# Kernel tuning notes

Measured on AMD Instinct MI355X. Metric: run time of the kernel, lower is better.

The kernel has to match this reference:

```python
import jax, jax.numpy as jnp
import numpy as np

# SofthebbArgs constants (rate, adaptive=True, p, dot_uw=False, temp)
RATE = 1e-3
TEMP = 1.0
P = 0.5


def negate_non_maximal(t):
    # keep the per-row max entry, negate all others
    idx = jnp.argmax(t, axis=-1)                      # [B]
    mask = idx[:, None] == jnp.arange(t.shape[-1])    # [B, OUT]
    return jnp.where(mask, t, -t)


def setup_inputs() -> dict:
    key = jax.random.key(0)
    k1, k2 = jax.random.split(key, 2)
    B, IN, OUT = 8192, 1024, 1024
    x = jax.random.normal(k1, (B, IN), dtype=jnp.float32)
    # xavier_normal_ with gain=1: std = sqrt(2/(fan_in+fan_out))
    W = jax.random.normal(k2, (OUT, IN), dtype=jnp.float32) * (2.0 / (IN + OUT)) ** 0.5
    b = jnp.zeros((OUT,), dtype=jnp.float32)
    return {"x": x, "W": W, "b": b}


def reference(x, W, b):
    # --- HebbianLinear.forward (act = Identity) ---
    u = x @ W.T + b                                   # [B, OUT]
    y = u
    # --- softhebb: y = softmax(y / temp), then _hebb with dot_uw=False ---
    ysm = jax.nn.softmax(y / TEMP, axis=1)
    yn = negate_non_maximal(ysm)                      # [B, OUT]
    Bn = x.shape[0]
    # _hebb materializes dw[b,o,i] = yn[b,o]*(x[b,i] - u[b,o]*W[o,i]) then means over b.
    # Algebraically fused (no [B,OUT,IN] intermediate):
    #   step[o,i] = (yn^T x)[o,i]/B - mean_b(yn[b,o]*u[b,o]) * W[o,i]
    step = (yn.T @ x) / Bn - jnp.mean(yn * u, axis=0)[:, None] * W  # [OUT, IN]
    # adaptive per-row rate: rate * |1 - ||W_row||_2|^p
    diff = jnp.abs(1.0 - jnp.linalg.norm(W, axis=1))  # [OUT]
    rate = RATE * diff ** P
    return rate[:, None] * step                       # [OUT, IN]
```

## Files before the change

kernel.cpp:

```cpp
#include <hip/hip_runtime.h>

#define BATCH 8192
#define INF_  1024
#define OUTF  1024
#define INV_B (1.0f/8192.0f)
#define RATE_C 1e-3f
#define SPLITZ 8

typedef __bf16 bf16x8 __attribute__((ext_vector_type(8)));
typedef float  f32x4  __attribute__((ext_vector_type(4)));
typedef float  f32x16 __attribute__((ext_vector_type(16)));
typedef const __attribute__((address_space(1))) unsigned int* gas_t;
typedef __attribute__((address_space(3))) unsigned int* las_t;

static __device__ __forceinline__ unsigned short f2bf(float f) {
  unsigned int u = __float_as_uint(f);
  u += 0x7fffu + ((u >> 16) & 1u);
  return (unsigned short)(u >> 16);
}
static __device__ __forceinline__ float bf2f(unsigned short h) {
  return __uint_as_float(((unsigned int)h) << 16);
}

__global__ __launch_bounds__(256) void k_convert(
    const float* __restrict__ x, unsigned short* __restrict__ xb,
    unsigned short* __restrict__ xT, const float* __restrict__ W,
    unsigned short* __restrict__ Wb, float* __restrict__ rate) {
  const int t = threadIdx.x;
  if (blockIdx.x >= 2048) {
    __shared__ float red[256];
    const int o = blockIdx.x - 2048;
    float4 v = *(const float4*)&W[(size_t)o * INF_ + t * 4];
    ushort4 h;
    h.x = f2bf(v.x); h.y = f2bf(v.y); h.z = f2bf(v.z); h.w = f2bf(v.w);
    *(ushort4*)&Wb[(size_t)o * INF_ + t * 4] = h;
    red[t] = v.x * v.x + v.y * v.y + v.z * v.z + v.w * v.w;
    __syncthreads();
    for (int s = 128; s > 0; s >>= 1) {
      if (t < s) red[t] += red[t + s];
      __syncthreads();
    }
    if (t == 0) {
      float nrm = sqrtf(red[0]);
      rate[o] = RATE_C * sqrtf(fabsf(1.0f - nrm));
    }
    return;
  }
  __shared__ unsigned int t32[64][33];
  const int bx = blockIdx.x & 15;
  const int by = blockIdx.x >> 4;
  const int r0 = by * 64;
  const int c0 = bx * 64;
  const int m = t & 15;
  const int q = t >> 4;
#pragma unroll
  for (int p = 0; p < 2; ++p) {
    const int r2 = p * 16 + q;
    const int b  = r0 + 2 * r2;
    float4 v0 = *(const float4*)&x[(size_t)b * INF_ + c0 + 4 * m];
    float4 v1 = *(const float4*)&x[(size_t)(b + 1) * INF_ + c0 + 4 * m];
    ushort4 h0, h1;
    h0.x = f2bf(v0.x); h0.y = f2bf(v0.y); h0.z = f2bf(v0.z); h0.w = f2bf(v0.w);
    h1.x = f2bf(v1.x); h1.y = f2bf(v1.y); h1.z = f2bf(v1.z); h1.w = f2bf(v1.w);
    *(ushort4*)&xb[(size_t)b * INF_ + c0 + 4 * m] = h0;
    *(ushort4*)&xb[(size_t)(b + 1) * INF_ + c0 + 4 * m] = h1;
    t32[4 * m + 0][r2] = (unsigned int)h0.x | ((unsigned int)h1.x << 16);
    t32[4 * m + 1][r2] = (unsigned int)h0.y | ((unsigned int)h1.y << 16);
    t32[4 * m + 2][r2] = (unsigned int)h0.z | ((unsigned int)h1.z << 16);
    t32[4 * m + 3][r2] = (unsigned int)h0.w | ((unsigned int)h1.w << 16);
  }
  __syncthreads();
  const int c  = t >> 2;
  const int sg = t & 3;
  unsigned int vb[8];
#pragma unroll
  for (int k = 0; k < 8; ++k) vb[k] = t32[c][sg * 8 + k];
  unsigned short* dst = &xT[(size_t)(c0 + c) * BATCH + r0 + sg * 16];
  *(uint4*)&dst[0] = make_uint4(vb[0], vb[1], vb[2], vb[3]);
  *(uint4*)&dst[8] = make_uint4(vb[4], vb[5], vb[6], vb[7]);
}

__global__ __launch_bounds__(256, 3) void k_gemm(
    const unsigned short* __restrict__ A, const unsigned short* __restrict__ B,
    int lda, int ldb, int kChunk, void* __restrict__ C, int ldc,
    const float* __restrict__ bias, int mode) {
  __shared__ unsigned short smem[128 * 132];
  unsigned short* As = smem;
  unsigned short* Bs = smem + 128 * 64;
  const int t  = threadIdx.x;
  const int id = blockIdx.x;
  int bx, by, bz;
  if (mode == 0) {
    by = (id & 7) | ((id >> 6) << 3);
    bx = (id >> 3) & 7;
    bz = 0;
  } else {
    bz = id & 7;
    by = (id >> 3) & 7;
    bx = (id >> 6) & 7;
  }
  const int m0   = by * 128;
  const int n0   = bx * 128;
  const int k0   = bz * kChunk;
  const int lane = t & 63;
  const int wave = t >> 6;
  const int sr   = lane >> 3;
  const int scx  = ((lane & 7) ^ sr) * 8;
  const int wm   = (wave >> 1) * 64;
  const int wn   = (wave & 1) * 64;
  const int fm   = lane & 31;
  const int fh   = lane >> 5;

  f32x16 acc[2][2] = {};

  const int ldsRow0 = wave * 8;
  const size_t gArow = (size_t)(m0 + ldsRow0 + sr) * lda + scx;
  const size_t gBrow = (size_t)(n0 + ldsRow0 + sr) * ldb + scx;

  for (int ks = 0; ks < kChunk; ks += 64) {
    const int k = k0 + ks;
#pragma unroll
    for (int j = 0; j < 4; ++j) {
      __builtin_amdgcn_global_load_lds(
          (gas_t)&A[gArow + (size_t)j * 32 * lda + k],
          (las_t)&As[(ldsRow0 + j * 32) * 64], 16, 0, 0);
      __builtin_amdgcn_global_load_lds(
          (gas_t)&B[gBrow + (size_t)j * 32 * ldb + k],
          (las_t)&Bs[(ldsRow0 + j * 32) * 64], 16, 0, 0);
    }
    __syncthreads();
#pragma unroll
    for (int kk = 0; kk < 64; kk += 16) {
      const int ckk = (kk >> 3) + fh;
      const int swz = (ckk ^ (lane & 7)) << 3;
      bf16x8 af[2], bf[2];
#pragma unroll
      for (int i = 0; i < 2; ++i)
        af[i] = *(const bf16x8*)&As[(wm + i * 32 + fm) * 64 + swz];
#pragma unroll
      for (int i = 0; i < 2; ++i)
        bf[i] = *(const bf16x8*)&Bs[(wn + i * 32 + fm) * 64 + swz];
#pragma unroll
      for (int mt = 0; mt < 2; ++mt)
#pragma unroll
        for (int nt = 0; nt < 2; ++nt)
          acc[mt][nt] = __builtin_amdgcn_mfma_f32_32x32x16_bf16(
              af[mt], bf[nt], acc[mt][nt], 0, 0, 0);
    }
    __syncthreads();
  }

#pragma unroll
  for (int nt = 0; nt < 2; ++nt) {
    const int cc = wn + nt * 32 + fm;
    const float bv = (mode == 0) ? bias[n0 + cc] : 0.0f;
#pragma unroll
    for (int mt = 0; mt < 2; ++mt) {
#pragma unroll
      for (int r = 0; r < 16; ++r) {
        const int rr = wm + mt * 32 + (r & 3) + 8 * (r >> 2) + 4 * fh;
        smem[rr * 132 + cc] = f2bf(acc[mt][nt][r] + bv);
      }
    }
  }
  __syncthreads();
  unsigned short* Cb = (mode == 0)
      ? (unsigned short*)C
      : (unsigned short*)C + (size_t)bz * (1024u * 1024u);
#pragma unroll
  for (int i = 0; i < 8; ++i) {
    const int row = i * 16 + (t >> 4);
    const int ch  = (t & 15) * 8;
    const unsigned short* src = &smem[row * 132 + ch];
    unsigned short* dst = &Cb[(size_t)(m0 + row) * ldc + n0 + ch];
    *(uint2*)&dst[0] = *(const uint2*)&src[0];
    *(uint2*)&dst[4] = *(const uint2*)&src[4];
  }
}

__global__ __launch_bounds__(256) void k_row_stats(
    const unsigned short* __restrict__ ub, const float* __restrict__ x,
    const float* __restrict__ W, float* __restrict__ rowmax,
    float* __restrict__ rowinv, int* __restrict__ rowarg) {
  __shared__ int cands[4][32];
  __shared__ int cnt[4];
  const int lane = threadIdx.x & 63;
  const int wave = threadIdx.x >> 6;
  const int b    = blockIdx.x * 4 + wave;
  const int oBase = lane * 16;

  float a[16];
  {
    uint4 q0 = *(const uint4*)&ub[(size_t)b * OUTF + oBase];
    uint4 q1 = *(const uint4*)&ub[(size_t)b * OUTF + oBase + 8];
    const unsigned int* qa = (const unsigned int*)&q0;
    const unsigned int* qb = (const unsigned int*)&q1;
#pragma unroll
    for (int c = 0; c < 4; ++c) {
      a[2 * c]         = __uint_as_float(qa[c] << 16);
      a[2 * c + 1]     = __uint_as_float(qa[c] & 0xffff0000u);
      a[8 + 2 * c]     = __uint_as_float(qb[c] << 16);
      a[8 + 2 * c + 1] = __uint_as_float(qb[c] & 0xffff0000u);
    }
  }
  float mv = a[0]; int mi = oBase;
#pragma unroll
  for (int j = 1; j < 16; ++j)
    if (a[j] > mv) { mv = a[j]; mi = oBase + j; }
#pragma unroll
  for (int off = 1; off < 64; off <<= 1) {
    float ov = __shfl_xor(mv, off);
    int   oi = __shfl_xor(mi, off);
    if (ov > mv || (ov == mv && oi < mi)) { mv = ov; mi = oi; }
  }
  const float M = mv;
  float se = 0.0f;
#pragma unroll
  for (int j = 0; j < 16; ++j) se += __expf(a[j] - M);
#pragma unroll
  for (int off = 1; off < 64; off <<= 1) se += __shfl_xor(se, off);

  const float thr = M - 0.10f;
  unsigned int cflags = 0;
  int ccount = 0;
#pragma unroll
  for (int j = 0; j < 16; ++j)
    if (a[j] >= thr) { cflags |= (1u << j); ++ccount; }
  int tot = ccount;
#pragma unroll
  for (int off = 1; off < 64; off <<= 1) tot += __shfl_xor(tot, off);

  int best = mi;
  if (tot > 1) {
    if (lane == 0) cnt[wave] = 0;
    for (int j = 0; j < 16; ++j)
      if (cflags & (1u << j)) {
        int p = atomicAdd(&cnt[wave], 1);
        if (p < 32) cands[wave][p] = oBase + j;
      }
    int nc = cnt[wave]; if (nc > 32) nc = 32;
    float xr[16];
    const float* xp = &x[(size_t)b * INF_ + oBase];
#pragma unroll
    for (int j = 0; j < 16; j += 4) {
      float4 v = *(const float4*)&xp[j];
      xr[j] = v.x; xr[j + 1] = v.y; xr[j + 2] = v.z; xr[j + 3] = v.w;
    }
    float bv = -3.4e38f; int bi = 0x7fffffff;
    for (int c = 0; c < nc; ++c) {
      const int o = cands[wave][c];
      const float* wp = &W[(size_t)o * INF_ + oBase];
      float d = 0.0f;
#pragma unroll
      for (int j = 0; j < 16; j += 4) {
        float4 v = *(const float4*)&wp[j];
        d += xr[j] * v.x + xr[j + 1] * v.y + xr[j + 2] * v.z +
             xr[j + 3] * v.w;
      }
#pragma unroll
      for (int off = 1; off < 64; off <<= 1) d += __shfl_xor(d, off);
      if (d > bv || (d == bv && o < bi)) { bv = d; bi = o; }
    }
    best = bi;
  }
  if (lane == 0) {
    rowmax[b] = M;
    rowinv[b] = 1.0f / se;
    rowarg[b] = best;
  }
}

__global__ __launch_bounds__(256) void k_yn(
    const unsigned short* __restrict__ ub, const float* __restrict__ rowmax,
    const float* __restrict__ rowinv, const int* __restrict__ rowarg,
    unsigned short* __restrict__ ynT, float* __restrict__ s_part) {
  __shared__ unsigned short tile[256][72];
  __shared__ float smax[64], sinv[64];
  __shared__ int   sarg[64];
  const int t  = threadIdx.x;
  const int o0 = blockIdx.x * 256;
  const int b0 = blockIdx.y * 64;
  if (t < 64) {
    smax[t] = rowmax[b0 + t];
    sinv[t] = rowinv[b0 + t];
    sarg[t] = rowarg[b0 + t];
  }
  __syncthreads();
  const int o = o0 + t;
  float sacc = 0.0f;
#pragma unroll
  for (int g = 0; g < 8; ++g) {
    uint4 pkv;
    unsigned short* pk = (unsigned short*)&pkv;
#pragma unroll
    for (int j = 0; j < 8; ++j) {
      const int r = g * 8 + j;
      float uu  = bf2f(ub[(size_t)(b0 + r) * OUTF + o]);
      float ysm = __expf(uu - smax[r]) * sinv[r];
      float yn  = (o == sarg[r]) ? ysm : -ysm;
      sacc += yn * uu;
      pk[j] = f2bf(yn);
    }
    *(uint4*)&tile[t][g * 8] = pkv;
  }
  s_part[(size_t)blockIdx.y * OUTF + o] = sacc;
  __syncthreads();
#pragma unroll
  for (int it = 0; it < 8; ++it) {
    const int row = it * 32 + (t >> 3);
    const int seg = (t & 7) * 8;
    uint4 vv = *(const uint4*)&tile[row][seg];
    *(uint4*)&ynT[(size_t)(o0 + row) * BATCH + b0 + seg] = vv;
  }
}

__global__ __launch_bounds__(256) void k_final(
    const unsigned short* __restrict__ Cp, const float* __restrict__ W,
    const float* __restrict__ s_part, const float* __restrict__ rate,
    float* __restrict__ out) {
  __shared__ float sred[128];
  const int t  = threadIdx.x;
  const int id = blockIdx.x;
  const int o  = ((id & 7) << 7) | (id >> 3);
  if (t < 128) sred[t] = s_part[(size_t)t * OUTF + o];
  __syncthreads();
  for (int s2 = 64; s2 > 0; s2 >>= 1) {
    if (t < s2) sred[t] += sred[t + s2];
    __syncthreads();
  }
  const float sb = sred[0] * INV_B;
  const float rt = rate[o];
  const int i0 = t * 4;
  float cx = 0, cy = 0, cz = 0, cw = 0;
#pragma unroll
  for (int z = 0; z < SPLITZ; ++z) {
    ushort4 h = *(const ushort4*)&Cp[(size_t)z * (1024u * 1024u) +
                                     (size_t)o * INF_ + i0];
    cx += bf2f(h.x); cy += bf2f(h.y); cz += bf2f(h.z); cw += bf2f(h.w);
  }
  float4 w = *(const float4*)&W[(size_t)o * INF_ + i0];
  float4 r;
  r.x = rt * (cx * INV_B - sb * w.x);
  r.y = rt * (cy * INV_B - sb * w.y);
  r.z = rt * (cz * INV_B - sb * w.z);
  r.w = rt * (cw * INV_B - sb * w.w);
  *(float4*)&out[(size_t)o * INF_ + i0] = r;
}

extern "C" void kernel_launch(void* const* d_in, const int* in_sizes, int n_in,
                              void* d_out, int out_size, void* d_ws, size_t ws_size,
                              hipStream_t stream) {
  const float* x    = (const float*)d_in[0];
  const float* W    = (const float*)d_in[1];
  const float* bias = (const float*)d_in[2];
  float* out = (float*)d_out;
  char* ws = (char*)d_ws;

  unsigned short* ub    = (unsigned short*)(ws + 0);
  unsigned short* xb    = (unsigned short*)(ws + 16777216);
  unsigned short* xT    = (unsigned short*)(ws + 33554432);
  unsigned short* ynT   = (unsigned short*)(ws + 50331648);
  unsigned short* Wb    = (unsigned short*)(ws + 67108864);
  float*          rate  = (float*)(ws + 69206016);
  float*          spart = (float*)(ws + 69210112);
  float*          rmax  = (float*)(ws + 69734400);
  float*          rinv  = (float*)(ws + 69767168);
  int*            rarg  = (int*)  (ws + 69799936);

  k_convert<<<dim3(3072), 256, 0, stream>>>(x, xb, xT, W, Wb, rate);
  k_gemm<<<dim3(512), 256, 0, stream>>>(xb, Wb, 1024, 1024, 1024,
                                        ub, 1024, bias, 0);
  k_row_stats<<<dim3(2048), 256, 0, stream>>>(ub, x, W, rmax, rinv, rarg);
  k_yn<<<dim3(4, 128), 256, 0, stream>>>(ub, rmax, rinv, rarg, ynT, spart);
  k_gemm<<<dim3(512), 256, 0, stream>>>(ynT, xT, 8192, 8192, 1024,
                                        ws, 1024, nullptr, 1);
  k_final<<<dim3(1024), 256, 0, stream>>>((const unsigned short*)ws, W, spart,
                                          rate, out);
}
```

Measured before the change: 153.6 us.

## Double-buffer LDS tiles in bf16 GEMM to overlap global loads with MFMA

The GEMM kernel now keeps two LDS buffers for the A/B tiles. It issues the global-to-LDS loads for the next K step right after the barrier, while MFMAs run on the current buffer. This removes one barrier per iteration and hides load latency behind compute. In exchange, LDS use per block doubles and the launch bound drops from 3 to 2 blocks per CU, which may lower occupancy. The epilogue staging area now spans both buffers.

Result: no change. 151.9 us, median of 2 (-1.1%).

```diff
diff --git a/kernel.cpp b/kernel.cpp
--- a/kernel.cpp
+++ b/kernel.cpp
@@ -80,13 +80,11 @@
   *(uint4*)&dst[8] = make_uint4(vb[4], vb[5], vb[6], vb[7]);
 }
 
-__global__ __launch_bounds__(256, 3) void k_gemm(
+__global__ __launch_bounds__(256, 2) void k_gemm(
     const unsigned short* __restrict__ A, const unsigned short* __restrict__ B,
     int lda, int ldb, int kChunk, void* __restrict__ C, int ldc,
     const float* __restrict__ bias, int mode) {
-  __shared__ unsigned short smem[128 * 132];
-  unsigned short* As = smem;
-  unsigned short* Bs = smem + 128 * 64;
+  __shared__ unsigned short smem[2][16384];
   const int t  = threadIdx.x;
   const int id = blockIdx.x;
   int bx, by, bz;
@@ -117,18 +115,33 @@
   const size_t gArow = (size_t)(m0 + ldsRow0 + sr) * lda + scx;
   const size_t gBrow = (size_t)(n0 + ldsRow0 + sr) * ldb + scx;
 
+#pragma unroll
+  for (int j = 0; j < 4; ++j) {
+    __builtin_amdgcn_global_load_lds(
+        (gas_t)&A[gArow + (size_t)j * 32 * lda + k0],
+        (las_t)&smem[0][(ldsRow0 + j * 32) * 64], 16, 0, 0);
+    __builtin_amdgcn_global_load_lds(
+        (gas_t)&B[gBrow + (size_t)j * 32 * ldb + k0],
+        (las_t)&smem[0][8192 + (ldsRow0 + j * 32) * 64], 16, 0, 0);
+  }
+
   for (int ks = 0; ks < kChunk; ks += 64) {
-    const int k = k0 + ks;
-#pragma unroll
-    for (int j = 0; j < 4; ++j) {
-      __builtin_amdgcn_global_load_lds(
-          (gas_t)&A[gArow + (size_t)j * 32 * lda + k],
-          (las_t)&As[(ldsRow0 + j * 32) * 64], 16, 0, 0);
-      __builtin_amdgcn_global_load_lds(
-          (gas_t)&B[gBrow + (size_t)j * 32 * ldb + k],
-          (las_t)&Bs[(ldsRow0 + j * 32) * 64], 16, 0, 0);
-    }
+    const int buf = (ks >> 6) & 1;
     __syncthreads();
+    if (ks + 64 < kChunk) {
+      const int kn = k0 + ks + 64;
+#pragma unroll
+      for (int j = 0; j < 4; ++j) {
+        __builtin_amdgcn_global_load_lds(
+            (gas_t)&A[gArow + (size_t)j * 32 * lda + kn],
+            (las_t)&smem[buf ^ 1][(ldsRow0 + j * 32) * 64], 16, 0, 0);
+        __builtin_amdgcn_global_load_lds(
+            (gas_t)&B[gBrow + (size_t)j * 32 * ldb + kn],
+            (las_t)&smem[buf ^ 1][8192 + (ldsRow0 + j * 32) * 64], 16, 0, 0);
+      }
+    }
+    const unsigned short* As = smem[buf];
+    const unsigned short* Bs = smem[buf] + 8192;
 #pragma unroll
     for (int kk = 0; kk < 64; kk += 16) {
       const int ckk = (kk >> 3) + fh;
@@ -147,9 +160,10 @@
           acc[mt][nt] = __builtin_amdgcn_mfma_f32_32x32x16_bf16(
               af[mt], bf[nt], acc[mt][nt], 0, 0, 0);
     }
-    __syncthreads();
-  }
-
+  }
+  __syncthreads();
+
+  unsigned short* ep = &smem[0][0];
 #pragma unroll
   for (int nt = 0; nt < 2; ++nt) {
     const int cc = wn + nt * 32 + fm;
@@ -159,7 +173,7 @@
 #pragma unroll
       for (int r = 0; r < 16; ++r) {
         const int rr = wm + mt * 32 + (r & 3) + 8 * (r >> 2) + 4 * fh;
-        smem[rr * 132 + cc] = f2bf(acc[mt][nt][r] + bv);
+        ep[rr * 132 + cc] = f2bf(acc[mt][nt][r] + bv);
       }
     }
   }
@@ -171,7 +185,7 @@
   for (int i = 0; i < 8; ++i) {
     const int row = i * 16 + (t >> 4);
     const int ch  = (t & 15) * 8;
-    const unsigned short* src = &smem[row * 132 + ch];
+    const unsigned short* src = &ep[row * 132 + ch];
     unsigned short* dst = &Cb[(size_t)(m0 + row) * ldc + n0 + ch];
     *(uint2*)&dst[0] = *(const uint2*)&src[0];
     *(uint2*)&dst[4] = *(const uint2*)&src[4];
```

## Double-buffer GEMM A tiles and register-prefetch B, shrink yn tiles

Applied to the files above, without the earlier changes.

The GEMM now double-buffers the A tile in LDS via async global-to-LDS loads and prefetches the next B tile into registers, writing it to a swizzled LDS slot at the start of each iteration. This is meant to overlap global memory latency with MFMA work instead of loading and then waiting. Separately, k_yn processes 32 batch rows per block instead of 64, doubling the grid, and each thread writes its own output row directly. k_final and the workspace layout are adjusted for the doubled s_part partials. LDS use per GEMM block changes and register pressure rises, which may affect occupancy under the 3-block launch bound.

New measurement: 207.5 us. 1.35x slower.

```diff
diff --git a/kernel.cpp b/kernel.cpp
--- a/kernel.cpp
+++ b/kernel.cpp
@@ -84,9 +84,7 @@
     const unsigned short* __restrict__ A, const unsigned short* __restrict__ B,
     int lda, int ldb, int kChunk, void* __restrict__ C, int ldc,
     const float* __restrict__ bias, int mode) {
-  __shared__ unsigned short smem[128 * 132];
-  unsigned short* As = smem;
-  unsigned short* Bs = smem + 128 * 64;
+  __shared__ unsigned short smem[24576];
   const int t  = threadIdx.x;
   const int id = blockIdx.x;
   int bx, by, bz;
@@ -115,20 +113,45 @@
 
   const int ldsRow0 = wave * 8;
   const size_t gArow = (size_t)(m0 + ldsRow0 + sr) * lda + scx;
-  const size_t gBrow = (size_t)(n0 + ldsRow0 + sr) * ldb + scx;
+
+  const int brow = t >> 1;
+  const int bc0  = (t & 1) * 4;
+  const size_t gBrow = (size_t)(n0 + brow) * ldb + bc0 * 8;
+  const int bre = brow & 7;
+
+#pragma unroll
+  for (int j = 0; j < 4; ++j)
+    __builtin_amdgcn_global_load_lds(
+        (gas_t)&A[gArow + (size_t)j * 32 * lda + k0],
+        (las_t)&smem[(ldsRow0 + j * 32) * 64], 16, 0, 0);
+  uint4 bv[4];
+#pragma unroll
+  for (int j = 0; j < 4; ++j)
+    bv[j] = *(const uint4*)&B[gBrow + (size_t)j * 8 + k0];
 
   for (int ks = 0; ks < kChunk; ks += 64) {
-    const int k = k0 + ks;
+    const int buf = (ks >> 6) & 1;
+    __syncthreads();
 #pragma unroll
     for (int j = 0; j < 4; ++j) {
-      __builtin_amdgcn_global_load_lds(
-          (gas_t)&A[gArow + (size_t)j * 32 * lda + k],
-          (las_t)&As[(ldsRow0 + j * 32) * 64], 16, 0, 0);
-      __builtin_amdgcn_global_load_lds(
-          (gas_t)&B[gBrow + (size_t)j * 32 * ldb + k],
-          (las_t)&Bs[(ldsRow0 + j * 32) * 64], 16, 0, 0);
+      const int dch = (bc0 + j) ^ bre;
+      *(uint4*)&smem[16384 + brow * 64 + dch * 8] = bv[j];
     }
     __syncthreads();
+    if (ks + 64 < kChunk) {
+      const int kn = k0 + ks + 64;
+#pragma unroll
+      for (int j = 0; j < 4; ++j)
+        __builtin_amdgcn_global_load_lds(
+            (gas_t)&A[gArow + (size_t)j * 32 * lda + kn],
+            (las_t)&smem[(buf ^ 1) * 8192 + (ldsRow0 + j * 32) * 64],
+            16, 0, 0);
+#pragma unroll
+      for (int j = 0; j < 4; ++j)
+        bv[j] = *(const uint4*)&B[gBrow + (size_t)j * 8 + kn];
+    }
+    const unsigned short* As = &smem[buf * 8192];
+    const unsigned short* Bs = &smem[16384];
 #pragma unroll
     for (int kk = 0; kk < 64; kk += 16) {
       const int ckk = (kk >> 3) + fh;
@@ -147,19 +170,19 @@
           acc[mt][nt] = __builtin_amdgcn_mfma_f32_32x32x16_bf16(
               af[mt], bf[nt], acc[mt][nt], 0, 0, 0);
     }
-    __syncthreads();
-  }
+  }
+  __syncthreads();
 
 #pragma unroll
   for (int nt = 0; nt < 2; ++nt) {
     const int cc = wn + nt * 32 + fm;
-    const float bv = (mode == 0) ? bias[n0 + cc] : 0.0f;
+    const float bvv = (mode == 0) ? bias[n0 + cc] : 0.0f;
 #pragma unroll
     for (int mt = 0; mt < 2; ++mt) {
 #pragma unroll
       for (int r = 0; r < 16; ++r) {
         const int rr = wm + mt * 32 + (r & 3) + 8 * (r >> 2) + 4 * fh;
-        smem[rr * 132 + cc] = f2bf(acc[mt][nt][r] + bv);
+        smem[rr * 132 + cc] = f2bf(acc[mt][nt][r] + bvv);
       }
     }
   }
@@ -274,13 +297,13 @@
     const unsigned short* __restrict__ ub, const float* __restrict__ rowmax,
     const float* __restrict__ rowinv, const int* __restrict__ rowarg,
     unsigned short* __restrict__ ynT, float* __restrict__ s_part) {
-  __shared__ unsigned short tile[256][72];
-  __shared__ float smax[64], sinv[64];
-  __shared__ int   sarg[64];
+  __shared__ unsigned short tile[256][40];
+  __shared__ float smax[32], sinv[32];
+  __shared__ int   sarg[32];
   const int t  = threadIdx.x;
   const int o0 = blockIdx.x * 256;
-  const int b0 = blockIdx.y * 64;
-  if (t < 64) {
+  const int b0 = blockIdx.y * 32;
+  if (t < 32) {
     smax[t] = rowmax[b0 + t];
     sinv[t] = rowinv[b0 + t];
     sarg[t] = rowarg[b0 + t];
@@ -289,7 +312,7 @@
   const int o = o0 + t;
   float sacc = 0.0f;
 #pragma unroll
-  for (int g = 0; g < 8; ++g) {
+  for (int g = 0; g < 4; ++g) {
     uint4 pkv;
     unsigned short* pk = (unsigned short*)&pkv;
 #pragma unroll
@@ -305,12 +328,11 @@
   }
   s_part[(size_t)blockIdx.y * OUTF + o] = sacc;
   __syncthreads();
-#pragma unroll
-  for (int it = 0; it < 8; ++it) {
-    const int row = it * 32 + (t >> 3);
-    const int seg = (t & 7) * 8;
-    uint4 vv = *(const uint4*)&tile[row][seg];
-    *(uint4*)&ynT[(size_t)(o0 + row) * BATCH + b0 + seg] = vv;
+  {
+    unsigned short* dst = &ynT[(size_t)o * BATCH + b0];
+#pragma unroll
+    for (int g = 0; g < 4; ++g)
+      *(uint4*)&dst[g * 8] = *(const uint4*)&tile[t][g * 8];
   }
 }
 
@@ -318,13 +340,13 @@
     const unsigned short* __restrict__ Cp, const float* __restrict__ W,
     const float* __restrict__ s_part, const float* __restrict__ rate,
     float* __restrict__ out) {
-  __shared__ float sred[128];
+  __shared__ float sred[256];
   const int t  = threadIdx.x;
   const int id = blockIdx.x;
   const int o  = ((id & 7) << 7) | (id >> 3);
-  if (t < 128) sred[t] = s_part[(size_t)t * OUTF + o];
-  __syncthreads();
-  for (int s2 = 64; s2 > 0; s2 >>= 1) {
+  sred[t] = s_part[(size_t)t * OUTF + o];
+  __syncthreads();
+  for (int s2 = 128; s2 > 0; s2 >>= 1) {
     if (t < s2) sred[t] += sred[t + s2];
     __syncthreads();
   }
@@ -363,15 +385,15 @@
   unsigned short* Wb    = (unsigned short*)(ws + 67108864);
   float*          rate  = (float*)(ws + 69206016);
   float*          spart = (float*)(ws + 69210112);
-  float*          rmax  = (float*)(ws + 69734400);
-  float*          rinv  = (float*)(ws + 69767168);
-  int*            rarg  = (int*)  (ws + 69799936);
+  float*          rmax  = (float*)(ws + 70258688);
+  float*          rinv  = (float*)(ws + 70291456);
+  int*            rarg  = (int*)  (ws + 70324224);
 
   k_convert<<<dim3(3072), 256, 0, stream>>>(x, xb, xT, W, Wb, rate);
   k_gemm<<<dim3(512), 256, 0, stream>>>(xb, Wb, 1024, 1024, 1024,
                                         ub, 1024, bias, 0);
   k_row_stats<<<dim3(2048), 256, 0, stream>>>(ub, x, W, rmax, rinv, rarg);
-  k_yn<<<dim3(4, 128), 256, 0, stream>>>(ub, rmax, rinv, rarg, ynT, spart);
+  k_yn<<<dim3(4, 256), 256, 0, stream>>>(ub, rmax, rinv, rarg, ynT, spart);
   k_gemm<<<dim3(512), 256, 0, stream>>>(ynT, xT, 8192, 8192, 1024,
                                         ws, 1024, nullptr, 1);
   k_final<<<dim3(1024), 256, 0, stream>>>((const unsigned short*)ws, W, spart,
```
